# Optimization experiments

Measured on AMD Instinct MI355X. Metric: run time of the kernel, lower is better.

The kernel has to match this reference:

```python
import jax, jax.numpy as jnp
import numpy as np
import math

DIM = 768
NUM_HEADS = 12
HEAD_DIM = DIM // NUM_HEADS


def setup_inputs() -> dict:
    key = jax.random.key(0)
    k_x, k_q, k_k, k_v = jax.random.split(key, 4)
    s = 1.0 / math.sqrt(DIM)
    return {
        "x": jax.random.normal(k_x, (2, 2048, DIM), dtype=jnp.float32),
        "Wq": jax.random.normal(k_q, (DIM, DIM), dtype=jnp.float32) * s,
        "Wk": jax.random.normal(k_k, (DIM, DIM), dtype=jnp.float32) * s,
        "Wv": jax.random.normal(k_v, (DIM, DIM), dtype=jnp.float32) * s,
    }


def reference(x, Wq, Wk, Wv):
    b, n, _ = x.shape
    # nn.Linear(dim, dim, bias=False): y = x @ W.T
    def split_heads(y):
        return y.reshape(b, n, NUM_HEADS, HEAD_DIM).transpose(0, 2, 1, 3)  # b h n d
    Q = split_heads(x @ Wq.T)
    K = split_heads(x @ Wk.T)
    V = split_heads(x @ Wv.T)
    scores = jnp.einsum('bhqd,bhkd->bhqk', Q, K)
    # FAITHFUL to source: softmax over the HEADS axis (dim=1), then scale by 1/sqrt(dim)
    attn = jax.nn.softmax(scores, axis=1) / math.sqrt(DIM)
    out = jnp.einsum('bhqk,bhkd->bhqd', attn, V)
    out = out.transpose(0, 2, 1, 3).reshape(b, n, DIM)  # b n (h d)
    return out  # to_out is Identity (project_out=False)
```

## Files before the change

kernel.cpp:

```cpp
#include <hip/hip_runtime.h>

#define DIM 768
#define NHEADS 12
#define HDIM 64
#define BATCH 2
#define SEQ 2048
#define ROWS (BATCH*SEQ)
#define KSPLIT 4

typedef __attribute__((ext_vector_type(8))) _Float16 f16x8;
typedef __attribute__((ext_vector_type(4))) _Float16 f16x4;
typedef __attribute__((ext_vector_type(2))) _Float16 f16x2;
typedef __attribute__((ext_vector_type(4))) float    f32x4;

__device__ __forceinline__ void dma16(const _Float16* g, _Float16* l) {
    __builtin_amdgcn_global_load_lds(
        (const __attribute__((address_space(1))) unsigned int*)g,
        (__attribute__((address_space(3))) unsigned int*)l, 16, 0, 0);
}


__global__ __launch_bounds__(256) void cvt_all(
    const float* __restrict__ x,  const float* __restrict__ wq,
    const float* __restrict__ wk, const float* __restrict__ wv,
    _Float16* __restrict__ xf,  _Float16* __restrict__ wqf,
    _Float16* __restrict__ wkf, _Float16* __restrict__ wvf)
{
    const int lane = threadIdx.x & 63;
    const int wid  = (blockIdx.x * 256 + threadIdx.x) >> 6;
    const float* src; _Float16* dst; int t;
    float sc = 1.0f;
    if (wid < 6144)      { src = x;  dst = xf;  t = wid;        }
    else if (wid < 7296) { src = wq; dst = wqf; t = wid - 6144; sc = 1.4426950408889634f; }
    else if (wid < 8448) { src = wk; dst = wkf; t = wid - 7296; }
    else                 { src = wv; dst = wvf; t = wid - 8448; }
    const int c = lane & 15, quad = lane >> 4;
    const int mt = t / 24, kt = t % 24;
    const float* p = src + (size_t)(mt*16 + c) * 768 + kt*32 + quad*8;
    float4 v0 = *(const float4*)p;
    float4 v1 = *(const float4*)(p + 4);
    f16x8 o;
    o[0]=(_Float16)(v0.x*sc); o[1]=(_Float16)(v0.y*sc); o[2]=(_Float16)(v0.z*sc); o[3]=(_Float16)(v0.w*sc);
    o[4]=(_Float16)(v1.x*sc); o[5]=(_Float16)(v1.y*sc); o[6]=(_Float16)(v1.z*sc); o[7]=(_Float16)(v1.w*sc);
    *reinterpret_cast<f16x8*>(dst + ((size_t)t * 64 + lane) * 8) = o;
}

__global__ __launch_bounds__(512) void gemm3(
    const _Float16* __restrict__ xf, const _Float16* __restrict__ wqkf,
    const _Float16* __restrict__ wvf,
    _Float16* __restrict__ Qf, _Float16* __restrict__ Kf, _Float16* __restrict__ Vkt)
{
    __shared__ _Float16 Ab[2][16*512];
    __shared__ _Float16 Bb[2][8*512];
    const int tid = threadIdx.x, lane = tid & 63, w = tid >> 6;
    const int c = lane & 15, quad = lane >> 4;

    const _Float16 *Af, *Bf;
    int mt0, nt0, mode;
    if ((int)blockIdx.x < 192) {
        int mt = blockIdx.x / 12, nt = blockIdx.x % 12;
        Af = xf; Bf = wqkf; mt0 = mt*16; nt0 = nt*8; mode = 0;
    } else {
        int v = blockIdx.x - 192;
        int mt = v / 32, nt = v % 32;
        Af = wvf; Bf = xf; mt0 = mt*16; nt0 = nt*8; mode = 1;
    }

    auto stage = [&](int kt, int buf) {
#pragma unroll
        for (int u = 0; u < 3; ++u) {
            const int cc = w*3 + u;
            const _Float16* s = (cc < 16) ? Af + ((size_t)(mt0+cc)*24 + kt)*512
                                          : Bf + ((size_t)(nt0+cc-16)*24 + kt)*512;
            _Float16* d = (cc < 16) ? &Ab[buf][cc*512] : &Bb[buf][(cc-16)*512];
            dma16(s + lane*8, d);
        }
    };

    stage(0, 0);
    __syncthreads();

    f32x4 acc[4][4] = {};
    for (int kt = 0; kt < 24; ++kt) {
        const int cur = kt & 1;
        if (kt < 23) stage(kt+1, cur^1);
        f16x8 a[4], b[4];
#pragma unroll
        for (int i = 0; i < 4; ++i)
            a[i] = *(const f16x8*)(&Ab[cur][((w>>1)*4 + i)*512] + lane*8);
#pragma unroll
        for (int j = 0; j < 4; ++j)
            b[j] = *(const f16x8*)(&Bb[cur][((w&1)*4 + j)*512] + lane*8);
#pragma unroll
        for (int i = 0; i < 4; ++i)
#pragma unroll
            for (int j = 0; j < 4; ++j)
                acc[i][j] = __builtin_amdgcn_mfma_f32_16x16x32_f16(a[i], b[j], acc[i][j], 0,0,0);
        __syncthreads();
    }

    _Float16* L = &Ab[0][0] + w*1280;
#pragma unroll
    for (int i2 = 0; i2 < 2; ++i2)
#pragma unroll
        for (int j2 = 0; j2 < 2; ++j2) {
#pragma unroll
            for (int ii = 0; ii < 2; ++ii)
#pragma unroll
                for (int jj = 0; jj < 2; ++jj)
#pragma unroll
                    for (int r = 0; r < 4; ++r)
                        L[(ii*16 + quad*4 + r)*40 + jj*16 + c] =
                            (_Float16)acc[i2*2+ii][j2*2+jj][r];
#pragma unroll
            for (int ii = 0; ii < 2; ++ii) {
                const int mtg = mt0 + (w>>1)*4 + i2*2 + ii;
                if (mode == 0) {
                    f16x8 v = *(const f16x8*)(L + (ii*16 + c)*40 + quad*8);
                    const int nt32 = (nt0 + (w&1)*4)/2 + j2;
                    _Float16* dst = (nt32 < 24)
                        ? Qf + ((size_t)(mtg*24 + nt32)*64 + lane)*8
                        : Kf + ((size_t)(mtg*24 + nt32 - 24)*64 + lane)*8;
                    *(f16x8*)dst = v;
                } else {
#pragma unroll
                    for (int jj = 0; jj < 2; ++jj) {
                        f16x4 v4 = *(const f16x4*)(L + (ii*16 + c)*40 + jj*16 + quad*4);
                        const int kcu = nt0 + (w&1)*4 + j2*2 + jj;
                        *(f16x4*)(Vkt + ((size_t)kcu*48 + mtg)*256 + lane*4) = v4;
                    }
                }
            }
        }
}

__global__ __launch_bounds__(512) __attribute__((amdgpu_waves_per_eu(4)))
void attn_kernel(
    const _Float16* __restrict__ Qf, const _Float16* __restrict__ Kf,
    const _Float16* __restrict__ Vkt,
    float* __restrict__ out,
    _Float16* __restrict__ part)
{
    __shared__ __attribute__((aligned(16))) _Float16 Kb[24*512];
    __shared__ __attribute__((aligned(16))) float    Ps[8][336];
    __shared__ __attribute__((aligned(16))) _Float16 Pl[2][12][16][20];
    const int tid = threadIdx.x, lane = tid & 63, w = tid >> 6;
    const int c = lane & 15, quad = lane >> 4;
    const int qi = w >> 2, g = w & 3;

    const int bid = blockIdx.x;
    const int qb = bid & 63;
    const int ks = (bid >> 6) & 3;
    const int b  = bid >> 8;
    const int qrow0 = b*SEQ + qb*32;
    const int qt16  = (qrow0 >> 4) + qi;
    const int kb16  = (b*SEQ + ks*(SEQ/KSPLIT)) >> 4;
    const int psoff = quad*84 + c*4;

    f16x8 qreg[6];
#pragma unroll
    for (int u = 0; u < 6; ++u)
        qreg[u] = *(const f16x8*)(Qf + ((size_t)(qt16*24 + g*6 + u)*64 + lane)*8);

    const _Float16* Vb0 = Vkt + ((size_t)kb16*48 + g)*256 + (size_t)lane*4;

#pragma unroll
    for (int u = 0; u < 3; ++u)
        dma16(Kf + ((size_t)kb16*24 + w*3 + u)*512 + lane*8, &Kb[(w*3+u)*512]);
    __syncthreads();

    f32x4 o_acc[12] = {};
    f16x4 vv[12];
    f32x4 e3[3];

    for (int t = 0; t < 32; ++t) {
#pragma unroll
        for (int hh = 0; hh < 3; ++hh) {
            f16x8 ka = *(const f16x8*)(&Kb[(g*6 + hh*2    )*512] + lane*8);
            f16x8 k2 = *(const f16x8*)(&Kb[(g*6 + hh*2 + 1)*512] + lane*8);
            f32x4 a = {};
            a = __builtin_amdgcn_mfma_f32_16x16x32_f16(ka, qreg[hh*2],   a, 0,0,0);
            a = __builtin_amdgcn_mfma_f32_16x16x32_f16(k2, qreg[hh*2+1], a, 0,0,0);
            f32x4 ee;
#pragma unroll
            for (int r = 0; r < 4; ++r) ee[r] = __builtin_amdgcn_exp2f(a[r]);
            e3[hh] = ee;
        }
        {
            f32x4 ps;
#pragma unroll
            for (int r = 0; r < 4; ++r) ps[r] = e3[0][r] + e3[1][r] + e3[2][r];
            *(f32x4*)&Ps[qi*4+g][psoff] = ps;
        }
        if (t > 0) {
#pragma unroll
            for (int h = 0; h < 12; ++h) {
                f16x4 pf = *(const f16x4*)&Pl[qi][h][c][quad*4];
                o_acc[h] = __builtin_amdgcn_mfma_f32_16x16x16f16(vv[h], pf, o_acc[h], 0,0,0);
            }
        }
        __syncthreads();
        if (t < 31) {
#pragma unroll
            for (int u = 0; u < 3; ++u)
                dma16(Kf + ((size_t)(kb16+t+1)*24 + w*3 + u)*512 + lane*8,
                      &Kb[(w*3+u)*512]);
        }
        {
            f32x4 s0 = *(const f32x4*)&Ps[qi*4+0][psoff];
            f32x4 s1 = *(const f32x4*)&Ps[qi*4+1][psoff];
            f32x4 s2 = *(const f32x4*)&Ps[qi*4+2][psoff];
            f32x4 s3 = *(const f32x4*)&Ps[qi*4+3][psoff];
            f32x4 inv;
#pragma unroll
            for (int r = 0; r < 4; ++r)
                inv[r] = __builtin_amdgcn_rcpf(
                    (s0[r]+s1[r]+s2[r]+s3[r]) * 27.712812921102035f);
#pragma unroll
            for (int hh = 0; hh < 3; ++hh) {
                f16x4 pw;
#pragma unroll
                for (int r = 0; r < 4; ++r) pw[r] = (_Float16)(e3[hh][r]*inv[r]);
                *(f16x4*)&Pl[qi][g*3+hh][c][quad*4] = pw;
            }
        }
#pragma unroll
        for (int h = 0; h < 12; ++h)
            vv[h] = *(const f16x4*)(Vb0 + ((size_t)t*48 + h*4)*256);
        __syncthreads();
    }
#pragma unroll
    for (int h = 0; h < 12; ++h) {
        f16x4 pf = *(const f16x4*)&Pl[qi][h][c][quad*4];
        o_acc[h] = __builtin_amdgcn_mfma_f32_16x16x16f16(vv[h], pf, o_acc[h], 0,0,0);
    }

    if (ks == 0) {
#pragma unroll
        for (int h = 0; h < 12; ++h)
            *(f32x4*)(out + (size_t)(qrow0 + qi*16 + c)*DIM + h*64 + g*16 + quad*4)
                = o_acc[h];
    } else {
        _Float16* dst = part + (size_t)(ks - 1) * ROWS * DIM;
#pragma unroll
        for (int h = 0; h < 12; ++h) {
            f16x4 v;
#pragma unroll
            for (int r = 0; r < 4; ++r) v[r] = (_Float16)o_acc[h][r];
            *(f16x4*)(dst + (size_t)(qrow0 + qi*16 + c)*DIM + h*64 + g*16 + quad*4) = v;
        }
    }
}

__global__ __launch_bounds__(256) void reduce_add4(
    float* __restrict__ out, const _Float16* __restrict__ part, int n4)
{
    int i = blockIdx.x * 256 + threadIdx.x;
    if (i >= n4) return;
    float4 o = reinterpret_cast<float4*>(out)[i];
    const size_t N = (size_t)ROWS * DIM;
#pragma unroll
    for (int p = 0; p < 3; ++p) {
        f16x4 v = reinterpret_cast<const f16x4*>(part + p * N)[i];
        o.x += (float)v[0]; o.y += (float)v[1]; o.z += (float)v[2]; o.w += (float)v[3];
    }
    reinterpret_cast<float4*>(out)[i] = o;
}

extern "C" void kernel_launch(void* const* d_in, const int* in_sizes, int n_in,
                              void* d_out, int out_size, void* d_ws, size_t ws_size,
                              hipStream_t stream)
{
    const float* x  = (const float*)d_in[0];
    const float* Wq = (const float*)d_in[1];
    const float* Wk = (const float*)d_in[2];
    const float* Wv = (const float*)d_in[3];

    _Float16* ws  = (_Float16*)d_ws;
    const size_t XS = (size_t)ROWS * DIM;
    const size_t WS = (size_t)DIM * DIM;
    _Float16* xf   = ws;
    _Float16* wqf  = xf  + XS;
    _Float16* wkf  = wqf + WS;
    _Float16* wvf  = wkf + WS;
    _Float16* Qf   = wvf + WS;
    _Float16* Kf   = Qf  + XS;
    _Float16* Vkt  = Kf  + XS;
    _Float16* part = Vkt + XS;

    cvt_all<<<2400, 256, 0, stream>>>(x, Wq, Wk, Wv, xf, wqf, wkf, wvf);
    gemm3<<<288, 512, 0, stream>>>(xf, wqf, wvf, Qf, Kf, Vkt);
    attn_kernel<<<BATCH * KSPLIT * 64, 512, 0, stream>>>(
        Qf, Kf, Vkt, (float*)d_out, part);
    reduce_add4<<<(int)(XS/4 + 255)/256, 256, 0, stream>>>(
        (float*)d_out, part, (int)(XS/4));
}
```

Before: 178.1 us.

## Rewrite QKV projection GEMM as per-wave tiles loading directly from global

Replaces the shared-memory, block-cooperative GEMM with one in which each wave computes its own output tile (64x96 for Q/K, 64x64 for V). Operands are loaded straight from global memory into registers with a two-stage register double buffer, and shared memory is used only for the output shuffle. This removes the per-k-step barriers and LDS staging, and the grid grows from 288 to 448 blocks of 256 threads. The cost is that operand tiles are no longer shared across waves, so L2/global traffic rises, and the larger accumulator and register buffers increase register pressure.

```diff
diff --git a/kernel.cpp b/kernel.cpp
--- a/kernel.cpp
+++ b/kernel.cpp
@@ -45,93 +45,150 @@
     *reinterpret_cast<f16x8*>(dst + ((size_t)t * 64 + lane) * 8) = o;
 }
 
-__global__ __launch_bounds__(512) void gemm3(
+__global__ __launch_bounds__(256) void gemm3(
     const _Float16* __restrict__ xf, const _Float16* __restrict__ wqkf,
     const _Float16* __restrict__ wvf,
     _Float16* __restrict__ Qf, _Float16* __restrict__ Kf, _Float16* __restrict__ Vkt)
 {
-    __shared__ _Float16 Ab[2][16*512];
-    __shared__ _Float16 Bb[2][8*512];
+    __shared__ _Float16 Lds[4*1280];
     const int tid = threadIdx.x, lane = tid & 63, w = tid >> 6;
     const int c = lane & 15, quad = lane >> 4;
-
-    const _Float16 *Af, *Bf;
-    int mt0, nt0, mode;
-    if ((int)blockIdx.x < 192) {
-        int mt = blockIdx.x / 12, nt = blockIdx.x % 12;
-        Af = xf; Bf = wqkf; mt0 = mt*16; nt0 = nt*8; mode = 0;
-    } else {
-        int v = blockIdx.x - 192;
-        int mt = v / 32, nt = v % 32;
-        Af = wvf; Bf = xf; mt0 = mt*16; nt0 = nt*8; mode = 1;
-    }
-
-    auto stage = [&](int kt, int buf) {
-#pragma unroll
-        for (int u = 0; u < 3; ++u) {
-            const int cc = w*3 + u;
-            const _Float16* s = (cc < 16) ? Af + ((size_t)(mt0+cc)*24 + kt)*512
-                                          : Bf + ((size_t)(nt0+cc-16)*24 + kt)*512;
-            _Float16* d = (cc < 16) ? &Ab[buf][cc*512] : &Bb[buf][(cc-16)*512];
-            dma16(s + lane*8, d);
-        }
-    };
-
-    stage(0, 0);
-    __syncthreads();
-
-    f32x4 acc[4][4] = {};
-    for (int kt = 0; kt < 24; ++kt) {
-        const int cur = kt & 1;
-        if (kt < 23) stage(kt+1, cur^1);
-        f16x8 a[4], b[4];
-#pragma unroll
-        for (int i = 0; i < 4; ++i)
-            a[i] = *(const f16x8*)(&Ab[cur][((w>>1)*4 + i)*512] + lane*8);
-#pragma unroll
-        for (int j = 0; j < 4; ++j)
-            b[j] = *(const f16x8*)(&Bb[cur][((w&1)*4 + j)*512] + lane*8);
-#pragma unroll
-        for (int i = 0; i < 4; ++i)
-#pragma unroll
-            for (int j = 0; j < 4; ++j)
-                acc[i][j] = __builtin_amdgcn_mfma_f32_16x16x32_f16(a[i], b[j], acc[i][j], 0,0,0);
-        __syncthreads();
-    }
-
-    _Float16* L = &Ab[0][0] + w*1280;
-#pragma unroll
-    for (int i2 = 0; i2 < 2; ++i2)
-#pragma unroll
-        for (int j2 = 0; j2 < 2; ++j2) {
-#pragma unroll
-            for (int ii = 0; ii < 2; ++ii)
-#pragma unroll
-                for (int jj = 0; jj < 2; ++jj)
-#pragma unroll
-                    for (int r = 0; r < 4; ++r)
-                        L[(ii*16 + quad*4 + r)*40 + jj*16 + c] =
-                            (_Float16)acc[i2*2+ii][j2*2+jj][r];
-#pragma unroll
-            for (int ii = 0; ii < 2; ++ii) {
-                const int mtg = mt0 + (w>>1)*4 + i2*2 + ii;
-                if (mode == 0) {
+    const int bid = blockIdx.x;
+    _Float16* L = &Lds[w*1280];
+
+    if (bid < 256) {
+        const int u = bid*4 + w;
+        const int mt64 = u >> 4, nt96 = u & 15;
+        const _Float16* Ab = xf   + (size_t)(mt64*4)*24*512 + (size_t)lane*8;
+        const _Float16* Bb = wqkf + (size_t)(nt96*6)*24*512 + (size_t)lane*8;
+
+        f32x4 acc[4][6] = {};
+        f16x8 a0[4], b0[6], a1[4], b1[6];
+        auto load0 = [&](int kt) {
+#pragma unroll
+            for (int i = 0; i < 4; ++i) a0[i] = *(const f16x8*)(Ab + ((size_t)(i*24 + kt))*512);
+#pragma unroll
+            for (int j = 0; j < 6; ++j) b0[j] = *(const f16x8*)(Bb + ((size_t)(j*24 + kt))*512);
+        };
+        auto load1 = [&](int kt) {
+#pragma unroll
+            for (int i = 0; i < 4; ++i) a1[i] = *(const f16x8*)(Ab + ((size_t)(i*24 + kt))*512);
+#pragma unroll
+            for (int j = 0; j < 6; ++j) b1[j] = *(const f16x8*)(Bb + ((size_t)(j*24 + kt))*512);
+        };
+        auto step0 = [&]() {
+#pragma unroll
+            for (int i = 0; i < 4; ++i)
+#pragma unroll
+                for (int j = 0; j < 6; ++j)
+                    acc[i][j] = __builtin_amdgcn_mfma_f32_16x16x32_f16(a0[i], b0[j], acc[i][j], 0,0,0);
+        };
+        auto step1 = [&]() {
+#pragma unroll
+            for (int i = 0; i < 4; ++i)
+#pragma unroll
+                for (int j = 0; j < 6; ++j)
+                    acc[i][j] = __builtin_amdgcn_mfma_f32_16x16x32_f16(a1[i], b1[j], acc[i][j], 0,0,0);
+        };
+
+        load0(0);
+        for (int kt = 0; kt < 24; kt += 2) {
+            load1(kt+1);
+            step0();
+            if (kt < 22) load0(kt+2);
+            step1();
+        }
+
+#pragma unroll
+        for (int i2 = 0; i2 < 2; ++i2)
+#pragma unroll
+            for (int j2 = 0; j2 < 3; ++j2) {
+#pragma unroll
+                for (int ii = 0; ii < 2; ++ii)
+#pragma unroll
+                    for (int jj = 0; jj < 2; ++jj)
+#pragma unroll
+                        for (int r = 0; r < 4; ++r)
+                            L[(ii*16 + quad*4 + r)*40 + jj*16 + c] =
+                                (_Float16)acc[i2*2+ii][j2*2+jj][r];
+#pragma unroll
+                for (int ii = 0; ii < 2; ++ii) {
+                    const int mtg = mt64*4 + i2*2 + ii;
                     f16x8 v = *(const f16x8*)(L + (ii*16 + c)*40 + quad*8);
-                    const int nt32 = (nt0 + (w&1)*4)/2 + j2;
+                    const int nt32 = nt96*3 + j2;
                     _Float16* dst = (nt32 < 24)
                         ? Qf + ((size_t)(mtg*24 + nt32)*64 + lane)*8
                         : Kf + ((size_t)(mtg*24 + nt32 - 24)*64 + lane)*8;
                     *(f16x8*)dst = v;
-                } else {
+                }
+            }
+    } else {
+        const int u = (bid - 256)*4 + w;
+        const int mtv = u >> 6, ntv = u & 63;
+        const _Float16* Ab = wvf + (size_t)(mtv*4)*24*512 + (size_t)lane*8;
+        const _Float16* Bb = xf  + (size_t)(ntv*4)*24*512 + (size_t)lane*8;
+
+        f32x4 acc[4][4] = {};
+        f16x8 a0[4], b0[4], a1[4], b1[4];
+        auto load0 = [&](int kt) {
+#pragma unroll
+            for (int i = 0; i < 4; ++i) a0[i] = *(const f16x8*)(Ab + ((size_t)(i*24 + kt))*512);
+#pragma unroll
+            for (int j = 0; j < 4; ++j) b0[j] = *(const f16x8*)(Bb + ((size_t)(j*24 + kt))*512);
+        };
+        auto load1 = [&](int kt) {
+#pragma unroll
+            for (int i = 0; i < 4; ++i) a1[i] = *(const f16x8*)(Ab + ((size_t)(i*24 + kt))*512);
+#pragma unroll
+            for (int j = 0; j < 4; ++j) b1[j] = *(const f16x8*)(Bb + ((size_t)(j*24 + kt))*512);
+        };
+        auto step0 = [&]() {
+#pragma unroll
+            for (int i = 0; i < 4; ++i)
+#pragma unroll
+                for (int j = 0; j < 4; ++j)
+                    acc[i][j] = __builtin_amdgcn_mfma_f32_16x16x32_f16(a0[i], b0[j], acc[i][j], 0,0,0);
+        };
+        auto step1 = [&]() {
+#pragma unroll
+            for (int i = 0; i < 4; ++i)
+#pragma unroll
+                for (int j = 0; j < 4; ++j)
+                    acc[i][j] = __builtin_amdgcn_mfma_f32_16x16x32_f16(a1[i], b1[j], acc[i][j], 0,0,0);
+        };
+
+        load0(0);
+        for (int kt = 0; kt < 24; kt += 2) {
+            load1(kt+1);
+            step0();
+            if (kt < 22) load0(kt+2);
+            step1();
+        }
+
+#pragma unroll
+        for (int i2 = 0; i2 < 2; ++i2)
+#pragma unroll
+            for (int j2 = 0; j2 < 2; ++j2) {
+#pragma unroll
+                for (int ii = 0; ii < 2; ++ii)
+#pragma unroll
+                    for (int jj = 0; jj < 2; ++jj)
+#pragma unroll
+                        for (int r = 0; r < 4; ++r)
+                            L[(ii*16 + quad*4 + r)*40 + jj*16 + c] =
+                                (_Float16)acc[i2*2+ii][j2*2+jj][r];
+#pragma unroll
+                for (int ii = 0; ii < 2; ++ii) {
+                    const int mtg = mtv*4 + i2*2 + ii;
 #pragma unroll
                     for (int jj = 0; jj < 2; ++jj) {
                         f16x4 v4 = *(const f16x4*)(L + (ii*16 + c)*40 + jj*16 + quad*4);
-                        const int kcu = nt0 + (w&1)*4 + j2*2 + jj;
+                        const int kcu = ntv*4 + j2*2 + jj;
                         *(f16x4*)(Vkt + ((size_t)kcu*48 + mtg)*256 + lane*4) = v4;
                     }
                 }
             }
-        }
+    }
 }
 
 __global__ __launch_bounds__(512) __attribute__((amdgpu_waves_per_eu(4)))
@@ -289,7 +346,7 @@
     _Float16* part = Vkt + XS;
 
     cvt_all<<<2400, 256, 0, stream>>>(x, Wq, Wk, Wv, xf, wqf, wkf, wvf);
-    gemm3<<<288, 512, 0, stream>>>(xf, wqf, wvf, Qf, Kf, Vkt);
+    gemm3<<<448, 256, 0, stream>>>(xf, wqf, wvf, Qf, Kf, Vkt);
     attn_kernel<<<BATCH * KSPLIT * 64, 512, 0, stream>>>(
         Qf, Kf, Vkt, (float*)d_out, part);
     reduce_add4<<<(int)(XS/4 + 255)/256, 256, 0, stream>>>(
```

Measured after the change: 185.6 us. 1.04x slower.
